# Kernel optimization log

Measured on AMD Instinct MI355X. Metric: run time of the kernel, lower is better.

## Reference

```python
import jax, jax.numpy as jnp
import numpy as np

DIM = 1024
N_HEADS = 16
HEAD_DIM = DIM // N_HEADS
COND_DIM = 1024
MLP_RATIO = 4
B, S = 4, 1024
LN_EPS = 1e-5


def _layer_norm(x, w):
    # F.layer_norm without affine bias, then * weight (per original LayerNorm)
    x32 = x.astype(jnp.float32)
    mu = jnp.mean(x32, axis=-1, keepdims=True)
    var = jnp.var(x32, axis=-1, keepdims=True)
    return (x32 - mu) * jax.lax.rsqrt(var + LN_EPS) * w


def _rope(t, cos, sin):
    # t: [b, s, h, d]; cos/sin: [s, d/2]; rotate-half convention
    d2 = t.shape[-1] // 2
    t1, t2 = t[..., :d2], t[..., d2:]
    c = cos[None, :, None, :]
    s = sin[None, :, None, :]
    return jnp.concatenate([t1 * c - t2 * s, t2 * c + t1 * s], axis=-1)


def setup_inputs() -> dict:
    key = jax.random.key(0)
    ks = jax.random.split(key, 12)
    inv_freq = 1.0 / (10000.0 ** (np.arange(0, HEAD_DIM, 2) / HEAD_DIM))
    ang = np.arange(S)[:, None] * inv_freq[None, :]
    return {
        "x": jax.random.normal(ks[0], (B, S, DIM), jnp.float32),
        "cos": jnp.asarray(np.cos(ang), jnp.float32),
        "sin": jnp.asarray(np.sin(ang), jnp.float32),
        "c": jax.random.normal(ks[1], (B, COND_DIM), jnp.float32),
        "w_ln1": jnp.ones((DIM,), jnp.float32),
        "w_ln2": jnp.ones((DIM,), jnp.float32),
        "w_qkv": jax.random.normal(ks[2], (DIM, 3 * DIM), jnp.float32) * 0.02,
        "w_attn_out": jax.random.normal(ks[3], (DIM, DIM), jnp.float32) * 0.02,
        "w_mlp1": jax.random.normal(ks[4], (DIM, MLP_RATIO * DIM), jnp.float32) * 0.02,
        "b_mlp1": jnp.zeros((MLP_RATIO * DIM,), jnp.float32),
        "w_mlp2": jax.random.normal(ks[5], (MLP_RATIO * DIM, DIM), jnp.float32) * 0.02,
        "b_mlp2": jnp.zeros((DIM,), jnp.float32),
        "w_ada": jax.random.normal(ks[6], (COND_DIM, 6 * DIM), jnp.float32) * 0.02,
        "b_ada": jax.random.normal(ks[7], (6 * DIM,), jnp.float32) * 0.02,
    }


def reference(x, cos, sin, c, w_ln1, w_ln2, w_qkv, w_attn_out,
              w_mlp1, b_mlp1, w_mlp2, b_mlp2, w_ada, b_ada):
    b, s, dim = x.shape
    # adaLN modulation: [b, 6*dim] -> six [b, 1, dim] chunks
    mod = (c @ w_ada + b_ada)[:, None, :]
    shift_msa, scale_msa, gate_msa, shift_mlp, scale_mlp, gate_mlp = jnp.split(mod, 6, axis=2)

    x_skip = x
    h = _layer_norm(x, w_ln1) * (1.0 + scale_msa) + shift_msa
    qkv = (h @ w_qkv).reshape(b, s, 3, N_HEADS, HEAD_DIM)
    q = _rope(qkv[:, :, 0], cos, sin)
    k = _rope(qkv[:, :, 1], cos, sin)
    v = qkv[:, :, 2]

    scale = 1.0 / jnp.sqrt(jnp.asarray(HEAD_DIM, x.dtype))
    scores = jnp.einsum('bshd,bthd->bhst', q, k) * scale  # [b,h,s,s]
    attn = jax.nn.softmax(scores, axis=-1)
    o = jnp.einsum('bhst,bthd->bshd', attn, v).reshape(b, s, dim)

    x = x_skip + gate_msa * (o @ w_attn_out)

    h2 = _layer_norm(x, w_ln2) * (1.0 + scale_mlp) + shift_mlp
    m = jax.nn.gelu(h2 @ w_mlp1 + b_mlp1, approximate=True) @ w_mlp2 + b_mlp2
    return x + gate_mlp * m
```

## Files before the change

kernel.cpp:

```cpp
#include <hip/hip_runtime.h>
#include <stdint.h>

typedef unsigned short u16;
typedef __bf16 bf16x8 __attribute__((ext_vector_type(8)));
typedef float f32x4 __attribute__((ext_vector_type(4)));

#define MOD6  6144

__device__ __forceinline__ float b2f(unsigned int u) {
    union { unsigned int i; float f; } z; z.i = u << 16; return z.f;
}
__device__ __forceinline__ u16 f2b(float f) {
    union { float f; unsigned int i; } z; z.f = f;
    unsigned int i = z.i;
    return (u16)((i + 0x7fffu + ((i >> 16) & 1u)) >> 16);
}
union U4 { uint4 u; u16 s[8]; };
union U2 { uint2 u; u16 s[4]; };
union B8 { bf16x8 v; unsigned int w[4]; };

__device__ __forceinline__ float ldf(const void* p, size_t i, int isbf) {
    if (isbf) return b2f(((const u16*)p)[i]);
    return ((const float*)p)[i];
}
__device__ __forceinline__ void load4(const void* p, size_t i, int isbf, float* v) {
    if (isbf) {
        U2 t; t.u = *(const uint2*)((const u16*)p + i);
#pragma unroll
        for (int e = 0; e < 4; e++) v[e] = b2f(t.s[e]);
    } else {
        float4 f = *(const float4*)((const float*)p + i);
        v[0] = f.x; v[1] = f.y; v[2] = f.z; v[3] = f.w;
    }
}

__device__ __forceinline__ void gld16(u16* lds, const u16* g) {
    __builtin_amdgcn_global_load_lds(
        (__attribute__((address_space(1))) void*)(g),
        (__attribute__((address_space(3))) void*)(lds), 16, 0, 0);
}

__global__ void detect_dtype(const unsigned int* __restrict__ w, int* __restrict__ flag) {
    if (threadIdx.x == 0 && blockIdx.x == 0)
        *flag = (w[0] == 0x3F803F80u) ? 1 : 0;
}

__global__ void transpose_any(const void* __restrict__ in, u16* __restrict__ out,
                              int K, int N, const int* __restrict__ flag) {
    const int isbf = *flag;
    __shared__ u16 tile[64][66];
    const int ntn = N >> 6;
    const int k0 = (blockIdx.x / ntn) << 6;
    const int n0 = (blockIdx.x % ntn) << 6;
    const int tid = threadIdx.x;
    const int r = tid >> 3;
    const int c = (tid & 7) * 8;
#pragma unroll
    for (int rr = 0; rr < 64; rr += 32) {
        const size_t base = (size_t)(k0 + r + rr) * N + n0 + c;
        u16* t = &tile[r + rr][c];
        if (isbf) {
            U4 v; v.u = *(const uint4*)((const u16*)in + base);
#pragma unroll
            for (int e = 0; e < 8; e++) t[e] = v.s[e];
        } else {
            float4 a = *(const float4*)((const float*)in + base);
            float4 b = *(const float4*)((const float*)in + base + 4);
            t[0] = f2b(a.x); t[1] = f2b(a.y); t[2] = f2b(a.z); t[3] = f2b(a.w);
            t[4] = f2b(b.x); t[5] = f2b(b.y); t[6] = f2b(b.z); t[7] = f2b(b.w);
        }
    }
    __syncthreads();
#pragma unroll
    for (int rr = 0; rr < 64; rr += 32) {
        U4 v;
#pragma unroll
        for (int e = 0; e < 8; e++) v.s[e] = tile[c + e][r + rr];
        *(uint4*)&out[(size_t)(n0 + r + rr) * K + k0 + c] = v.u;
    }
}

__global__ void ada_partial(const void* __restrict__ c, const void* __restrict__ w_ada,
                            float* __restrict__ part, const int* __restrict__ flag) {
    const int isbf = *flag;
    const int g = blockIdx.x * 256 + threadIdx.x;
    const int slice = g / 24576;
    const int idx = g - slice * 24576;
    const int b = idx / MOD6, n = idx - (idx / MOD6) * MOD6;
    const int k0 = slice * 128;
    float acc = 0.f;
    if (isbf) {
        const u16* cr = (const u16*)c + b * 1024 + k0;
        const u16* wp = (const u16*)w_ada + (size_t)k0 * MOD6 + n;
#pragma unroll 8
        for (int k = 0; k < 128; k++)
            acc += b2f(cr[k]) * b2f(wp[(size_t)k * MOD6]);
    } else {
        const float* cr = (const float*)c + b * 1024 + k0;
        const float* wp = (const float*)w_ada + (size_t)k0 * MOD6 + n;
#pragma unroll 8
        for (int k = 0; k < 128; k++)
            acc += cr[k] * wp[(size_t)k * MOD6];
    }
    part[g] = acc;
}
__global__ void ada_reduce(const float* __restrict__ part, const void* __restrict__ b_ada,
                           float* __restrict__ mod, const int* __restrict__ flag) {
    const int g = blockIdx.x * 256 + threadIdx.x;
    float acc = ldf(b_ada, g % MOD6, *flag);
#pragma unroll
    for (int s = 0; s < 8; s++) acc += part[s * 24576 + g];
    mod[g] = acc;
}

__global__ void ln_mod_kernel(const void* __restrict__ x, const void* __restrict__ w,
                              const float* __restrict__ mod, int shift_off,
                              int scale_off, u16* __restrict__ out,
                              const int* __restrict__ flag, int x_is_f32) {
    const int isbf = *flag;
    const int xb = x_is_f32 ? 0 : isbf;
    const int tk = blockIdx.x;
    const int b = tk >> 10;
    const int tid = threadIdx.x;
    float v[4];
    load4(x, (size_t)tk * 1024 + tid * 4, xb, v);
    float s = v[0] + v[1] + v[2] + v[3];
    float ss = v[0]*v[0] + v[1]*v[1] + v[2]*v[2] + v[3]*v[3];
#pragma unroll
    for (int off = 1; off < 64; off <<= 1) {
        s  += __shfl_xor(s, off);
        ss += __shfl_xor(ss, off);
    }
    __shared__ float ls[4], lss[4];
    if ((tid & 63) == 0) { ls[tid >> 6] = s; lss[tid >> 6] = ss; }
    __syncthreads();
    s  = ls[0] + ls[1] + ls[2] + ls[3];
    ss = lss[0] + lss[1] + lss[2] + lss[3];
    const float mu  = s * (1.f / 1024.f);
    const float var = ss * (1.f / 1024.f) - mu * mu;
    const float rstd = rsqrtf(var + 1e-5f);
    float wv[4];
    load4(w, (size_t)tid * 4, isbf, wv);
    const float* mb = mod + (size_t)b * MOD6;
    U2 o;
#pragma unroll
    for (int e = 0; e < 4; e++) {
        const int col = tid * 4 + e;
        float n = (v[e] - mu) * rstd * wv[e];
        o.s[e] = f2b(n * (1.f + mb[scale_off + col]) + mb[shift_off + col]);
    }
    *(uint2*)(out + (size_t)tk * 1024 + tid * 4) = o.u;
}

__global__ void out_init(const float* __restrict__ res, const float* __restrict__ gate,
                         const void* __restrict__ bias, float* __restrict__ out,
                         const int* __restrict__ flag) {
    const int isbf = *flag;
    const int g = blockIdx.x * 256 + threadIdx.x;
    const int col = (g & 255) * 4;
    const int row = g >> 8;
    const int b = row >> 10;
    float bv[4];
    load4(bias, (size_t)col, isbf, bv);
    const float* gp = gate + (size_t)b * MOD6 + col;
    float4 r = *(const float4*)(res + (size_t)row * 1024 + col);
    float4 o;
    o.x = r.x + gp[0] * bv[0];
    o.y = r.y + gp[1] * bv[1];
    o.z = r.z + gp[2] * bv[2];
    o.w = r.w + gp[3] * bv[3];
    *(float4*)(out + (size_t)row * 1024 + col) = o;
}

#define EPI_STORE 0
#define EPI_RES_GATE 1
#define EPI_GELU_BIAS 2
#define EPI_RES_GATE_BIAS 3
#define EPI_ATOMIC_GATE 4

template <int EPI>
__launch_bounds__(256, 2)
__global__ void gemm_bt(const u16* __restrict__ A, const u16* __restrict__ Bt,
                        void* __restrict__ Cv, int M, int N, int K,
                        const void* __restrict__ res, const float* __restrict__ gate,
                        const void* __restrict__ bias, const int* __restrict__ flag,
                        int Ks) {
    __shared__ __align__(16) u16 sA[2][128 * 32];
    __shared__ __align__(16) u16 sB[2][128 * 32];
    const int isbf = flag ? *flag : 0;
    const int tid = threadIdx.x;
    const int lane = tid & 63;
    const int w = tid >> 6;
    const int wm = w >> 1, wn = w & 1;
    const int c16 = lane & 15, quad = lane >> 4;

    int bx, by, bz;
    {
        const int nx = gridDim.x, ny = gridDim.y, nz = gridDim.z;
        const int flat = blockIdx.x + nx * (blockIdx.y + ny * blockIdx.z);
        const int q = flat & 7;
        const int s = flat >> 3;
        const int g = s / nx;
        bx = s - g * nx;
        const int p = q * ((ny * nz) >> 3) + g;
        by = p % ny;
        bz = p / ny;
    }
    const int m0 = by * 128, n0 = bx * 128;
    const int kt0 = bz * Ks;

    const int srow = lane >> 2;
    const int schunk = lane & 3;
    const int gchunk = schunk ^ (srow & 3);

    const u16* gA = A + (size_t)m0 * K + 8 * gchunk + kt0;
    const u16* gB = Bt + (size_t)n0 * K + 8 * gchunk + kt0;
    const int cs = quad ^ (c16 & 3);

    const int r0 = 16 * w + srow;
    const int r1 = r0 + 64;
    const int d0 = r0 * 32 + 8 * schunk;
    const int d1 = r1 * 32 + 8 * schunk;

    f32x4 acc[4][4];
#pragma unroll
    for (int i = 0; i < 4; i++)
#pragma unroll
        for (int j = 0; j < 4; j++) acc[i][j] = (f32x4){0.f, 0.f, 0.f, 0.f};

    gld16(&sA[0][d0], gA + (size_t)r0 * K);
    gld16(&sB[0][d0], gB + (size_t)r0 * K);
    gld16(&sA[0][d1], gA + (size_t)r1 * K);
    gld16(&sB[0][d1], gB + (size_t)r1 * K);
    __syncthreads();

    const int nt = Ks >> 5;
    int cur = 0;
#pragma unroll 1
    for (int t = 0; t < nt; ++t) {
        if (t + 1 < nt) {
            const int kt = (t + 1) << 5;
            u16* dA = &sA[cur ^ 1][0];
            u16* dB = &sB[cur ^ 1][0];
            gld16(dA + d0, gA + (size_t)r0 * K + kt);
            gld16(dB + d0, gB + (size_t)r0 * K + kt);
            gld16(dA + d1, gA + (size_t)r1 * K + kt);
            gld16(dB + d1, gB + (size_t)r1 * K + kt);
        }
        const u16* fA = &sA[cur][0];
        const u16* fB = &sB[cur][0];
        bf16x8 af[4], bfr[4];
#pragma unroll
        for (int i = 0; i < 4; i++)
            af[i] = *(const bf16x8*)&fA[(64 * wm + 16 * i + c16) * 32 + 8 * cs];
#pragma unroll
        for (int j = 0; j < 4; j++)
            bfr[j] = *(const bf16x8*)&fB[(64 * wn + 16 * j + c16) * 32 + 8 * cs];
#pragma unroll
        for (int i = 0; i < 4; i++)
#pragma unroll
            for (int j = 0; j < 4; j++)
                acc[i][j] = __builtin_amdgcn_mfma_f32_16x16x32_bf16(
                    af[i], bfr[j], acc[i][j], 0, 0, 0);
        __syncthreads();
        cur ^= 1;
    }

#pragma unroll
    for (int i = 0; i < 4; i++) {
#pragma unroll
        for (int r = 0; r < 4; r++) {
            const int row = m0 + 64 * wm + 16 * i + 4 * quad + r;
            const int b = row >> 10;
#pragma unroll
            for (int j = 0; j < 4; j++) {
                const int col = n0 + 64 * wn + 16 * j + c16;
                float v = acc[i][j][r];
                if constexpr (EPI == EPI_GELU_BIAS) {
                    v += ldf(bias, col, isbf);
                    const float u = 0.7978845608f * (v + 0.044715f * v * v * v);
                    const float e = __expf(2.f * u);
                    const float t = 1.f - 2.f / (e + 1.f);
                    v = 0.5f * v * (1.f + t);
                } else if constexpr (EPI == EPI_RES_GATE) {
                    v = ldf(res, (size_t)row * N + col, isbf)
                        + gate[(size_t)b * MOD6 + col] * v;
                } else if constexpr (EPI == EPI_RES_GATE_BIAS) {
                    v += ldf(bias, col, isbf);
                    v = ((const float*)res)[(size_t)row * N + col]
                        + gate[(size_t)b * MOD6 + col] * v;
                }
                if constexpr (EPI == EPI_ATOMIC_GATE) {
                    atomicAdd((float*)Cv + (size_t)row * N + col,
                              gate[(size_t)b * MOD6 + col] * v);
                } else if constexpr (EPI == EPI_RES_GATE || EPI == EPI_RES_GATE_BIAS) {
                    ((float*)Cv)[(size_t)row * N + col] = v;
                } else {
                    ((u16*)Cv)[(size_t)row * N + col] = f2b(v);
                }
            }
        }
    }
}

__global__ void rope_kernel(u16* __restrict__ qkv, const void* __restrict__ cosb,
                            const void* __restrict__ sinb, const int* __restrict__ flag) {
    const int isbf = *flag;
    const int g = blockIdx.x * 256 + threadIdx.x;
    const int q8 = g & 7;
    const int h = (g >> 3) & 15;
    const int tk = g >> 7;
    const int s = tk & 1023;
    const int d = q8 * 4;
    u16* row = qkv + (size_t)tk * 3072;

    float c4[4], s4[4];
    load4(cosb, (size_t)s * 32 + d, isbf, c4);
    load4(sinb, (size_t)s * 32 + d, isbf, s4);

#pragma unroll
    for (int which = 0; which < 2; which++) {
        u16* p1 = row + which * 1024 + h * 64 + d;
        u16* p2 = p1 + 32;
        U2 t1, t2;
        t1.u = *(const uint2*)p1;
        t2.u = *(const uint2*)p2;
        U2 o1, o2;
#pragma unroll
        for (int e = 0; e < 4; e++) {
            const float a = b2f(t1.s[e]), bb = b2f(t2.s[e]);
            o1.s[e] = f2b(a * c4[e] - bb * s4[e]);
            o2.s[e] = f2b(bb * c4[e] + a * s4[e]);
        }
        *(uint2*)p1 = o1.u;
        *(uint2*)p2 = o2.u;
    }
}

__launch_bounds__(256, 4)
__global__ void attn_mfma(const u16* __restrict__ qkv, u16* __restrict__ o_out) {
    __shared__ __align__(16) u16 sK[64 * 72];
    __shared__ __align__(16) u16 sVt[64 * 72];
    const int flat = blockIdx.x;
    const int xq = flat & 7, xs = flat >> 3;
    const int qt = xs & 15;
    const int bh = xq * 8 + (xs >> 4);
    const int b = bh >> 4, h = bh & 15;
    const int tid = threadIdx.x;
    const int w = tid >> 6;
    const int lane = tid & 63;
    const int c = lane & 15;
    const int quad = lane >> 4;

    const int q0 = qt * 64 + w * 16;
    bf16x8 qf0, qf1;
    {
        const u16* qrow = qkv + (size_t)(b * 1024 + q0 + c) * 3072 + h * 64;
        qf0 = *(const bf16x8*)(qrow + quad * 8);
        qf1 = *(const bf16x8*)(qrow + 32 + quad * 8);
    }
    f32x4 of[4];
#pragma unroll
    for (int dt = 0; dt < 4; dt++) of[dt] = (f32x4){0.f, 0.f, 0.f, 0.f};
    float mI = -1e30f, lI = 0.f;

    const int skey = tid >> 3;
    const int sch  = tid & 7;
    const int src0 = (((2 * quad) & 3) << 4) + c;
    const int src1 = (((2 * quad + 1) & 3) << 4) + c;

#pragma unroll 1
    for (int kt = 0; kt < 1024; kt += 64) {
        __syncthreads();
#pragma unroll
        for (int p = 0; p < 2; p++) {
            const int key = skey + p * 32;
            const u16* krow = qkv + (size_t)(b * 1024 + kt + key) * 3072 + 1024
                              + h * 64 + sch * 8;
            uint4 kv = *(const uint4*)krow;
            *(uint4*)&sK[key * 72 + sch * 8] = kv;
            U4 vv; vv.u = *(const uint4*)(krow + 1024);
#pragma unroll
            for (int e = 0; e < 8; e++) sVt[(sch * 8 + e) * 72 + key] = vv.s[e];
        }
        __syncthreads();
#pragma unroll
        for (int ks = 0; ks < 64; ks += 32) {
            bf16x8 k00 = *(const bf16x8*)&sK[(ks + c) * 72 + quad * 8];
            bf16x8 k01 = *(const bf16x8*)&sK[(ks + c) * 72 + 32 + quad * 8];
            bf16x8 k10 = *(const bf16x8*)&sK[(ks + 16 + c) * 72 + quad * 8];
            bf16x8 k11 = *(const bf16x8*)&sK[(ks + 16 + c) * 72 + 32 + quad * 8];
            f32x4 s0 = (f32x4){0.f, 0.f, 0.f, 0.f};
            f32x4 s1 = (f32x4){0.f, 0.f, 0.f, 0.f};
            s0 = __builtin_amdgcn_mfma_f32_16x16x32_bf16(k00, qf0, s0, 0, 0, 0);
            s0 = __builtin_amdgcn_mfma_f32_16x16x32_bf16(k01, qf1, s0, 0, 0, 0);
            s1 = __builtin_amdgcn_mfma_f32_16x16x32_bf16(k10, qf0, s1, 0, 0, 0);
            s1 = __builtin_amdgcn_mfma_f32_16x16x32_bf16(k11, qf1, s1, 0, 0, 0);
            float sc[8];
#pragma unroll
            for (int r = 0; r < 4; r++) { sc[r] = s0[r] * 0.125f; sc[4 + r] = s1[r] * 0.125f; }
            float tm = sc[0];
#pragma unroll
            for (int j = 1; j < 8; j++) tm = fmaxf(tm, sc[j]);
            tm = fmaxf(tm, __shfl_xor(tm, 16));
            tm = fmaxf(tm, __shfl_xor(tm, 32));
            const float mNew = fmaxf(mI, tm);
            const float alpha = __expf(mI - mNew);
            float p8[8];
            float psum = 0.f;
#pragma unroll
            for (int j = 0; j < 8; j++) { p8[j] = __expf(sc[j] - mNew); psum += p8[j]; }
            psum += __shfl_xor(psum, 16);
            psum += __shfl_xor(psum, 32);
            lI = lI * alpha + psum;
            mI = mNew;
#pragma unroll
            for (int dt = 0; dt < 4; dt++) {
#pragma unroll
                for (int r = 0; r < 4; r++) of[dt][r] *= alpha;
            }
            const unsigned int a0 = (unsigned)f2b(p8[0]) | ((unsigned)f2b(p8[1]) << 16);
            const unsigned int a1 = (unsigned)f2b(p8[2]) | ((unsigned)f2b(p8[3]) << 16);
            const unsigned int b0 = (unsigned)f2b(p8[4]) | ((unsigned)f2b(p8[5]) << 16);
            const unsigned int b1 = (unsigned)f2b(p8[6]) | ((unsigned)f2b(p8[7]) << 16);
            const unsigned int xa0 = (unsigned)__shfl((int)a0, src0);
            const unsigned int xb0 = (unsigned)__shfl((int)b0, src0);
            const unsigned int xa1 = (unsigned)__shfl((int)a1, src0);
            const unsigned int xb1 = (unsigned)__shfl((int)b1, src0);
            const unsigned int ya0 = (unsigned)__shfl((int)a0, src1);
            const unsigned int yb0 = (unsigned)__shfl((int)b0, src1);
            const unsigned int ya1 = (unsigned)__shfl((int)a1, src1);
            const unsigned int yb1 = (unsigned)__shfl((int)b1, src1);
            B8 pf;
            pf.w[0] = quad < 2 ? xa0 : xb0;
            pf.w[1] = quad < 2 ? xa1 : xb1;
            pf.w[2] = quad < 2 ? ya0 : yb0;
            pf.w[3] = quad < 2 ? ya1 : yb1;
#pragma unroll
            for (int dt = 0; dt < 4; dt++) {
                bf16x8 vf = *(const bf16x8*)&sVt[(dt * 16 + c) * 72 + ks + quad * 8];
                of[dt] = __builtin_amdgcn_mfma_f32_16x16x32_bf16(vf, pf.v, of[dt], 0, 0, 0);
            }
        }
    }
    const float inv = 1.f / lI;
    const size_t orow = (size_t)(b * 1024 + q0 + c) * 1024 + h * 64;
#pragma unroll
    for (int dt = 0; dt < 4; dt++) {
        U2 pk;
#pragma unroll
        for (int r = 0; r < 4; r++) pk.s[r] = f2b(of[dt][r] * inv);
        *(uint2*)(o_out + orow + dt * 16 + quad * 4) = pk.u;
    }
}

extern "C" void kernel_launch(void* const* d_in, const int* in_sizes, int n_in,
                              void* d_out, int out_size, void* d_ws, size_t ws_size,
                              hipStream_t stream) {
    (void)in_sizes; (void)n_in; (void)out_size; (void)ws_size;
    const void* x      = d_in[0];
    const void* cosb   = d_in[1];
    const void* sinb   = d_in[2];
    const void* c      = d_in[3];
    const void* w_ln1  = d_in[4];
    const void* w_ln2  = d_in[5];
    const void* w_qkv  = d_in[6];
    const void* w_attn = d_in[7];
    const void* w_mlp1 = d_in[8];
    const void* b_mlp1 = d_in[9];
    const void* w_mlp2 = d_in[10];
    const void* b_mlp2 = d_in[11];
    const void* w_ada  = d_in[12];
    const void* b_ada  = d_in[13];
    char* ws = (char*)d_ws;

    u16*   wT_qkv  = (u16*)(ws + 0);
    u16*   wT_attn = (u16*)(ws + 6291456);
    u16*   wT_mlp1 = (u16*)(ws + 8388608);
    u16*   wT_mlp2 = (u16*)(ws + 16777216);
    float* mod     = (float*)(ws + 25165824);
    u16*   hbuf    = (u16*)(ws + 25264128);
    u16*   big     = (u16*)(ws + 33652736);
    float* x2      = (float*)(ws + 67207168);
    int*   flag    = (int*)(ws + 83984384);
    float* part    = (float*)big;

    detect_dtype<<<1, 64, 0, stream>>>((const unsigned int*)w_ln1, flag);
    transpose_any<<<dim3(16 * 48), 256, 0, stream>>>(w_qkv, wT_qkv, 1024, 3072, flag);
    transpose_any<<<dim3(16 * 16), 256, 0, stream>>>(w_attn, wT_attn, 1024, 1024, flag);
    transpose_any<<<dim3(16 * 64), 256, 0, stream>>>(w_mlp1, wT_mlp1, 1024, 4096, flag);
    transpose_any<<<dim3(64 * 16), 256, 0, stream>>>(w_mlp2, wT_mlp2, 4096, 1024, flag);
    ada_partial<<<768, 256, 0, stream>>>(c, w_ada, part, flag);
    ada_reduce<<<96, 256, 0, stream>>>(part, b_ada, mod, flag);
    ln_mod_kernel<<<4096, 256, 0, stream>>>(x, w_ln1, mod, 0, 1024, hbuf, flag, 0);
    gemm_bt<EPI_STORE><<<dim3(24, 32), 256, 0, stream>>>(
        hbuf, wT_qkv, big, 4096, 3072, 1024, nullptr, nullptr, nullptr, flag, 1024);
    rope_kernel<<<2048, 256, 0, stream>>>(big, cosb, sinb, flag);
    attn_mfma<<<1024, 256, 0, stream>>>(big, hbuf);
    gemm_bt<EPI_RES_GATE><<<dim3(8, 32), 256, 0, stream>>>(
        hbuf, wT_attn, x2, 4096, 1024, 1024, x, mod + 2048, nullptr, flag, 1024);
    ln_mod_kernel<<<4096, 256, 0, stream>>>(x2, w_ln2, mod, 3072, 4096, hbuf, flag, 1);
    out_init<<<4096, 256, 0, stream>>>(x2, mod + 5120, b_mlp2, (float*)d_out, flag);
    gemm_bt<EPI_GELU_BIAS><<<dim3(32, 32), 256, 0, stream>>>(
        hbuf, wT_mlp1, big, 4096, 4096, 1024, nullptr, nullptr, b_mlp1, flag, 1024);
    gemm_bt<EPI_ATOMIC_GATE><<<dim3(8, 32, 4), 256, 0, stream>>>(
        big, wT_mlp2, (float*)d_out, 4096, 1024, 4096, nullptr, mod + 5120, nullptr,
        flag, 1024);
}
```

Before: 460.6 us.

## Enlarge GEMM tiles to 256x256 with 512 threads; split-K attn-out projection

The shared bf16 GEMM now uses 256x256 output tiles computed by 8 waves (each wave 128x64), doubling LDS buffers and per-wave accumulators. The aim is to raise arithmetic intensity and cut global/LDS traffic per MFMA. The attention output projection switches from a fused residual+gate store to a copy of x into x2 followed by a 4-way split-K atomic-add GEMM, so the smaller-N GEMM gets more blocks. The cost is higher register pressure (128 accumulator floats per lane), fewer blocks for grid coverage on the large GEMMs, an extra copy kernel, and float atomics.

```diff
diff --git a/kernel.cpp b/kernel.cpp
--- a/kernel.cpp
+++ b/kernel.cpp
@@ -172,26 +172,34 @@
     *(float4*)(out + (size_t)row * 1024 + col) = o;
 }
 
+__global__ void copy_f32(const void* __restrict__ x, float* __restrict__ out,
+                         const int* __restrict__ flag) {
+    const int isbf = *flag;
+    const int g = blockIdx.x * 256 + threadIdx.x;
+    float v[4];
+    load4(x, (size_t)g * 4, isbf, v);
+    float4 o; o.x = v[0]; o.y = v[1]; o.z = v[2]; o.w = v[3];
+    *(float4*)(out + (size_t)g * 4) = o;
+}
+
 #define EPI_STORE 0
-#define EPI_RES_GATE 1
 #define EPI_GELU_BIAS 2
-#define EPI_RES_GATE_BIAS 3
 #define EPI_ATOMIC_GATE 4
 
 template <int EPI>
-__launch_bounds__(256, 2)
+__launch_bounds__(512, 2)
 __global__ void gemm_bt(const u16* __restrict__ A, const u16* __restrict__ Bt,
                         void* __restrict__ Cv, int M, int N, int K,
                         const void* __restrict__ res, const float* __restrict__ gate,
                         const void* __restrict__ bias, const int* __restrict__ flag,
                         int Ks) {
-    __shared__ __align__(16) u16 sA[2][128 * 32];
-    __shared__ __align__(16) u16 sB[2][128 * 32];
+    __shared__ __align__(16) u16 sA[2][256 * 32];
+    __shared__ __align__(16) u16 sB[2][256 * 32];
     const int isbf = flag ? *flag : 0;
     const int tid = threadIdx.x;
     const int lane = tid & 63;
     const int w = tid >> 6;
-    const int wm = w >> 1, wn = w & 1;
+    const int wm = w >> 2, wn = w & 3;
     const int c16 = lane & 15, quad = lane >> 4;
 
     int bx, by, bz;
@@ -206,31 +214,31 @@
         by = p % ny;
         bz = p / ny;
     }
-    const int m0 = by * 128, n0 = bx * 128;
+    const int m0 = by * 256, n0 = bx * 256;
     const int kt0 = bz * Ks;
 
-    const int srow = lane >> 2;
-    const int schunk = lane & 3;
+    const int srow = tid >> 2;
+    const int schunk = tid & 3;
     const int gchunk = schunk ^ (srow & 3);
 
     const u16* gA = A + (size_t)m0 * K + 8 * gchunk + kt0;
     const u16* gB = Bt + (size_t)n0 * K + 8 * gchunk + kt0;
     const int cs = quad ^ (c16 & 3);
 
-    const int r0 = 16 * w + srow;
-    const int r1 = r0 + 64;
+    const int r0 = srow;
+    const int r1 = srow + 128;
     const int d0 = r0 * 32 + 8 * schunk;
     const int d1 = r1 * 32 + 8 * schunk;
 
-    f32x4 acc[4][4];
-#pragma unroll
-    for (int i = 0; i < 4; i++)
+    f32x4 acc[8][4];
+#pragma unroll
+    for (int i = 0; i < 8; i++)
 #pragma unroll
         for (int j = 0; j < 4; j++) acc[i][j] = (f32x4){0.f, 0.f, 0.f, 0.f};
 
     gld16(&sA[0][d0], gA + (size_t)r0 * K);
+    gld16(&sA[0][d1], gA + (size_t)r1 * K);
     gld16(&sB[0][d0], gB + (size_t)r0 * K);
-    gld16(&sA[0][d1], gA + (size_t)r1 * K);
     gld16(&sB[0][d1], gB + (size_t)r1 * K);
     __syncthreads();
 
@@ -243,21 +251,21 @@
             u16* dA = &sA[cur ^ 1][0];
             u16* dB = &sB[cur ^ 1][0];
             gld16(dA + d0, gA + (size_t)r0 * K + kt);
+            gld16(dA + d1, gA + (size_t)r1 * K + kt);
             gld16(dB + d0, gB + (size_t)r0 * K + kt);
-            gld16(dA + d1, gA + (size_t)r1 * K + kt);
             gld16(dB + d1, gB + (size_t)r1 * K + kt);
         }
         const u16* fA = &sA[cur][0];
         const u16* fB = &sB[cur][0];
-        bf16x8 af[4], bfr[4];
-#pragma unroll
-        for (int i = 0; i < 4; i++)
-            af[i] = *(const bf16x8*)&fA[(64 * wm + 16 * i + c16) * 32 + 8 * cs];
+        bf16x8 af[8], bfr[4];
+#pragma unroll
+        for (int i = 0; i < 8; i++)
+            af[i] = *(const bf16x8*)&fA[(128 * wm + 16 * i + c16) * 32 + 8 * cs];
 #pragma unroll
         for (int j = 0; j < 4; j++)
             bfr[j] = *(const bf16x8*)&fB[(64 * wn + 16 * j + c16) * 32 + 8 * cs];
 #pragma unroll
-        for (int i = 0; i < 4; i++)
+        for (int i = 0; i < 8; i++)
 #pragma unroll
             for (int j = 0; j < 4; j++)
                 acc[i][j] = __builtin_amdgcn_mfma_f32_16x16x32_bf16(
@@ -267,10 +275,10 @@
     }
 
 #pragma unroll
-    for (int i = 0; i < 4; i++) {
+    for (int i = 0; i < 8; i++) {
 #pragma unroll
         for (int r = 0; r < 4; r++) {
-            const int row = m0 + 64 * wm + 16 * i + 4 * quad + r;
+            const int row = m0 + 128 * wm + 16 * i + 4 * quad + r;
             const int b = row >> 10;
 #pragma unroll
             for (int j = 0; j < 4; j++) {
@@ -282,19 +290,10 @@
                     const float e = __expf(2.f * u);
                     const float t = 1.f - 2.f / (e + 1.f);
                     v = 0.5f * v * (1.f + t);
-                } else if constexpr (EPI == EPI_RES_GATE) {
-                    v = ldf(res, (size_t)row * N + col, isbf)
-                        + gate[(size_t)b * MOD6 + col] * v;
-                } else if constexpr (EPI == EPI_RES_GATE_BIAS) {
-                    v += ldf(bias, col, isbf);
-                    v = ((const float*)res)[(size_t)row * N + col]
-                        + gate[(size_t)b * MOD6 + col] * v;
                 }
                 if constexpr (EPI == EPI_ATOMIC_GATE) {
                     atomicAdd((float*)Cv + (size_t)row * N + col,
                               gate[(size_t)b * MOD6 + col] * v);
-                } else if constexpr (EPI == EPI_RES_GATE || EPI == EPI_RES_GATE_BIAS) {
-                    ((float*)Cv)[(size_t)row * N + col] = v;
                 } else {
                     ((u16*)Cv)[(size_t)row * N + col] = f2b(v);
                 }
@@ -493,17 +492,18 @@
     ada_partial<<<768, 256, 0, stream>>>(c, w_ada, part, flag);
     ada_reduce<<<96, 256, 0, stream>>>(part, b_ada, mod, flag);
     ln_mod_kernel<<<4096, 256, 0, stream>>>(x, w_ln1, mod, 0, 1024, hbuf, flag, 0);
-    gemm_bt<EPI_STORE><<<dim3(24, 32), 256, 0, stream>>>(
+    gemm_bt<EPI_STORE><<<dim3(12, 16), 512, 0, stream>>>(
         hbuf, wT_qkv, big, 4096, 3072, 1024, nullptr, nullptr, nullptr, flag, 1024);
     rope_kernel<<<2048, 256, 0, stream>>>(big, cosb, sinb, flag);
     attn_mfma<<<1024, 256, 0, stream>>>(big, hbuf);
-    gemm_bt<EPI_RES_GATE><<<dim3(8, 32), 256, 0, stream>>>(
-        hbuf, wT_attn, x2, 4096, 1024, 1024, x, mod + 2048, nullptr, flag, 1024);
+    copy_f32<<<4096, 256, 0, stream>>>(x, x2, flag);
+    gemm_bt<EPI_ATOMIC_GATE><<<dim3(4, 16, 4), 512, 0, stream>>>(
+        hbuf, wT_attn, x2, 4096, 1024, 1024, nullptr, mod + 2048, nullptr, flag, 256);
     ln_mod_kernel<<<4096, 256, 0, stream>>>(x2, w_ln2, mod, 3072, 4096, hbuf, flag, 1);
     out_init<<<4096, 256, 0, stream>>>(x2, mod + 5120, b_mlp2, (float*)d_out, flag);
-    gemm_bt<EPI_GELU_BIAS><<<dim3(32, 32), 256, 0, stream>>>(
+    gemm_bt<EPI_GELU_BIAS><<<dim3(16, 16), 512, 0, stream>>>(
         hbuf, wT_mlp1, big, 4096, 4096, 1024, nullptr, nullptr, b_mlp1, flag, 1024);
-    gemm_bt<EPI_ATOMIC_GATE><<<dim3(8, 32, 4), 256, 0, stream>>>(
+    gemm_bt<EPI_ATOMIC_GATE><<<dim3(4, 16, 4), 512, 0, stream>>>(
         big, wT_mlp2, (float*)d_out, 4096, 1024, 4096, nullptr, mod + 5120, nullptr,
         flag, 1024);
 }
```

After: 535.1 us. 1.16x slower.

## Add 256x256-tile GEMM with 512 threads for split-K MLP2 projection

Applied to the files above, without the earlier changes.

Adds a second GEMM kernel using 256x256 output tiles, 8 waves of 512 threads, and 32x4 MFMA tiles per wave. It is used for the MLP down-projection with split-K of 8 (Ks=512) instead of 128x128 tiles with split-K 4. The goal is to raise arithmetic intensity and cut global and LDS traffic per FLOP. The cost is more atomic adds into the output (8 partials per element), higher register pressure from 32 accumulators per wave, and only 512 blocks.

```diff
diff --git a/kernel.cpp b/kernel.cpp
--- a/kernel.cpp
+++ b/kernel.cpp
@@ -175,16 +175,15 @@
 #define EPI_STORE 0
 #define EPI_RES_GATE 1
 #define EPI_GELU_BIAS 2
-#define EPI_RES_GATE_BIAS 3
 #define EPI_ATOMIC_GATE 4
 
 template <int EPI>
 __launch_bounds__(256, 2)
-__global__ void gemm_bt(const u16* __restrict__ A, const u16* __restrict__ Bt,
-                        void* __restrict__ Cv, int M, int N, int K,
-                        const void* __restrict__ res, const float* __restrict__ gate,
-                        const void* __restrict__ bias, const int* __restrict__ flag,
-                        int Ks) {
+__global__ void gemm128_bt(const u16* __restrict__ A, const u16* __restrict__ Bt,
+                           void* __restrict__ Cv, int M, int N, int K,
+                           const void* __restrict__ res, const float* __restrict__ gate,
+                           const void* __restrict__ bias, const int* __restrict__ flag,
+                           int Ks) {
     __shared__ __align__(16) u16 sA[2][128 * 32];
     __shared__ __align__(16) u16 sB[2][128 * 32];
     const int isbf = flag ? *flag : 0;
@@ -285,16 +284,128 @@
                 } else if constexpr (EPI == EPI_RES_GATE) {
                     v = ldf(res, (size_t)row * N + col, isbf)
                         + gate[(size_t)b * MOD6 + col] * v;
-                } else if constexpr (EPI == EPI_RES_GATE_BIAS) {
-                    v += ldf(bias, col, isbf);
-                    v = ((const float*)res)[(size_t)row * N + col]
-                        + gate[(size_t)b * MOD6 + col] * v;
                 }
                 if constexpr (EPI == EPI_ATOMIC_GATE) {
                     atomicAdd((float*)Cv + (size_t)row * N + col,
                               gate[(size_t)b * MOD6 + col] * v);
-                } else if constexpr (EPI == EPI_RES_GATE || EPI == EPI_RES_GATE_BIAS) {
+                } else if constexpr (EPI == EPI_RES_GATE) {
                     ((float*)Cv)[(size_t)row * N + col] = v;
+                } else {
+                    ((u16*)Cv)[(size_t)row * N + col] = f2b(v);
+                }
+            }
+        }
+    }
+}
+
+template <int EPI>
+__launch_bounds__(512, 2)
+__global__ void gemm256_bt(const u16* __restrict__ A, const u16* __restrict__ Bt,
+                           void* __restrict__ Cv, int M, int N, int K,
+                           const void* __restrict__ res, const float* __restrict__ gate,
+                           const void* __restrict__ bias, const int* __restrict__ flag,
+                           int Ks) {
+    __shared__ __align__(16) u16 sA[2][256 * 32];
+    __shared__ __align__(16) u16 sB[2][256 * 32];
+    const int isbf = flag ? *flag : 0;
+    const int tid = threadIdx.x;
+    const int lane = tid & 63;
+    const int w = tid >> 6;
+    const int wm = w >> 2, wn = w & 3;
+    const int c16 = lane & 15, quad = lane >> 4;
+
+    int bx, by, bz;
+    {
+        const int nx = gridDim.x, ny = gridDim.y, nz = gridDim.z;
+        const int flat = blockIdx.x + nx * (blockIdx.y + ny * blockIdx.z);
+        const int q = flat & 7;
+        const int s = flat >> 3;
+        const int g = s / nx;
+        bx = s - g * nx;
+        const int p = q * ((ny * nz) >> 3) + g;
+        by = p % ny;
+        bz = p / ny;
+    }
+    const int m0 = by * 256, n0 = bx * 256;
+    const int kt0 = bz * Ks;
+
+    const int srow = tid >> 2;
+    const int schunk = tid & 3;
+    const int gchunk = schunk ^ (srow & 3);
+
+    const u16* gA = A + (size_t)m0 * K + 8 * gchunk + kt0;
+    const u16* gB = Bt + (size_t)n0 * K + 8 * gchunk + kt0;
+    const int cs = quad ^ (c16 & 3);
+
+    const int r0 = srow;
+    const int r1 = srow + 128;
+    const int d0 = r0 * 32 + 8 * schunk;
+    const int d1 = r1 * 32 + 8 * schunk;
+
+    f32x4 acc[8][4];
+#pragma unroll
+    for (int i = 0; i < 8; i++)
+#pragma unroll
+        for (int j = 0; j < 4; j++) acc[i][j] = (f32x4){0.f, 0.f, 0.f, 0.f};
+
+    gld16(&sA[0][d0], gA + (size_t)r0 * K);
+    gld16(&sA[0][d1], gA + (size_t)r1 * K);
+    gld16(&sB[0][d0], gB + (size_t)r0 * K);
+    gld16(&sB[0][d1], gB + (size_t)r1 * K);
+    __syncthreads();
+
+    const int nt = Ks >> 5;
+    int cur = 0;
+#pragma unroll 1
+    for (int t = 0; t < nt; ++t) {
+        if (t + 1 < nt) {
+            const int kt = (t + 1) << 5;
+            u16* dA = &sA[cur ^ 1][0];
+            u16* dB = &sB[cur ^ 1][0];
+            gld16(dA + d0, gA + (size_t)r0 * K + kt);
+            gld16(dA + d1, gA + (size_t)r1 * K + kt);
+            gld16(dB + d0, gB + (size_t)r0 * K + kt);
+            gld16(dB + d1, gB + (size_t)r1 * K + kt);
+        }
+        const u16* fA = &sA[cur][0];
+        const u16* fB = &sB[cur][0];
+        bf16x8 af[8], bfr[4];
+#pragma unroll
+        for (int i = 0; i < 8; i++)
+            af[i] = *(const bf16x8*)&fA[(128 * wm + 16 * i + c16) * 32 + 8 * cs];
+#pragma unroll
+        for (int j = 0; j < 4; j++)
+            bfr[j] = *(const bf16x8*)&fB[(64 * wn + 16 * j + c16) * 32 + 8 * cs];
+#pragma unroll
+        for (int i = 0; i < 8; i++)
+#pragma unroll
+            for (int j = 0; j < 4; j++)
+                acc[i][j] = __builtin_amdgcn_mfma_f32_16x16x32_bf16(
+                    af[i], bfr[j], acc[i][j], 0, 0, 0);
+        __syncthreads();
+        cur ^= 1;
+    }
+
+#pragma unroll
+    for (int i = 0; i < 8; i++) {
+#pragma unroll
+        for (int r = 0; r < 4; r++) {
+            const int row = m0 + 128 * wm + 16 * i + 4 * quad + r;
+            const int b = row >> 10;
+#pragma unroll
+            for (int j = 0; j < 4; j++) {
+                const int col = n0 + 64 * wn + 16 * j + c16;
+                float v = acc[i][j][r];
+                if constexpr (EPI == EPI_GELU_BIAS) {
+                    v += ldf(bias, col, isbf);
+                    const float u = 0.7978845608f * (v + 0.044715f * v * v * v);
+                    const float e = __expf(2.f * u);
+                    const float t = 1.f - 2.f / (e + 1.f);
+                    v = 0.5f * v * (1.f + t);
+                }
+                if constexpr (EPI == EPI_ATOMIC_GATE) {
+                    atomicAdd((float*)Cv + (size_t)row * N + col,
+                              gate[(size_t)b * MOD6 + col] * v);
                 } else {
                     ((u16*)Cv)[(size_t)row * N + col] = f2b(v);
                 }
@@ -493,17 +604,17 @@
     ada_partial<<<768, 256, 0, stream>>>(c, w_ada, part, flag);
     ada_reduce<<<96, 256, 0, stream>>>(part, b_ada, mod, flag);
     ln_mod_kernel<<<4096, 256, 0, stream>>>(x, w_ln1, mod, 0, 1024, hbuf, flag, 0);
-    gemm_bt<EPI_STORE><<<dim3(24, 32), 256, 0, stream>>>(
+    gemm128_bt<EPI_STORE><<<dim3(24, 32), 256, 0, stream>>>(
         hbuf, wT_qkv, big, 4096, 3072, 1024, nullptr, nullptr, nullptr, flag, 1024);
     rope_kernel<<<2048, 256, 0, stream>>>(big, cosb, sinb, flag);
     attn_mfma<<<1024, 256, 0, stream>>>(big, hbuf);
-    gemm_bt<EPI_RES_GATE><<<dim3(8, 32), 256, 0, stream>>>(
+    gemm128_bt<EPI_RES_GATE><<<dim3(8, 32), 256, 0, stream>>>(
         hbuf, wT_attn, x2, 4096, 1024, 1024, x, mod + 2048, nullptr, flag, 1024);
     ln_mod_kernel<<<4096, 256, 0, stream>>>(x2, w_ln2, mod, 3072, 4096, hbuf, flag, 1);
     out_init<<<4096, 256, 0, stream>>>(x2, mod + 5120, b_mlp2, (float*)d_out, flag);
-    gemm_bt<EPI_GELU_BIAS><<<dim3(32, 32), 256, 0, stream>>>(
+    gemm128_bt<EPI_GELU_BIAS><<<dim3(32, 32), 256, 0, stream>>>(
         hbuf, wT_mlp1, big, 4096, 4096, 1024, nullptr, nullptr, b_mlp1, flag, 1024);
-    gemm_bt<EPI_ATOMIC_GATE><<<dim3(8, 32, 4), 256, 0, stream>>>(
+    gemm256_bt<EPI_ATOMIC_GATE><<<dim3(4, 16, 8), 512, 0, stream>>>(
         big, wT_mlp2, (float*)d_out, 4096, 1024, 4096, nullptr, mod + 5120, nullptr,
-        flag, 1024);
-}
+        flag, 512);
+}
```

Result: slower. 515.5 us (+11.9%).
